# Kernel tuning notes

Measured on AMD Instinct MI355X. Metric: run time of the kernel, lower is better.

The kernel has to match this reference:

```python
import jax, jax.numpy as jnp
import numpy as np

DIM = 128
HEADS = 8
K_RATIO = 0.5
LAYER_SCALE = 0.1
EPS = 1e-6


def setup_inputs() -> dict:
    key = jax.random.key(0)
    ks = jax.random.split(key, 18)
    d = DIM
    hd3 = d * 3  # high-frequency channels (lh,hl,hh)
    f = lambda k, shape, s=0.05: jax.random.normal(k, shape, dtype=jnp.float32) * s
    return {
        "x": jax.random.normal(ks[0], (8, d, 64, 64), dtype=jnp.float32),
        "qkv_w": f(ks[1], (3 * d, d)),
        "proj_w": f(ks[2], (d, d)),
        "attn_gn_g": 1.0 + f(ks[3], (d,)),
        "attn_gn_b": f(ks[4], (d,)),
        "he_dw_w": f(ks[5], (hd3, 1, 3, 3)),
        "he_gn1_g": 1.0 + f(ks[6], (hd3,)),
        "he_gn1_b": f(ks[7], (hd3,)),
        "he_pw_w": f(ks[8], (hd3, hd3)),
        "he_gn2_g": 1.0 + f(ks[9], (hd3,)),
        "he_gn2_b": f(ks[10], (hd3,)),
        "alpha": jnp.array([0.1], dtype=jnp.float32),
        "ffn_w1": f(ks[11], (2 * d, d)),
        "ffn_gn1_g": 1.0 + f(ks[12], (2 * d,)),
        "ffn_gn1_b": f(ks[13], (2 * d,)),
        "ffn_w2": f(ks[14], (d, 2 * d)),
        "ffn_gn2_g": 1.0 + f(ks[15], (d,)),
        "ffn_gn2_b": f(ks[16], (d,)),
    }


def _group_norm(x, g, b, groups):
    B, C, H, W = x.shape
    xg = x.reshape(B, groups, -1)
    mu = xg.mean(-1, keepdims=True)
    var = xg.var(-1, keepdims=True)
    xn = ((xg - mu) * jax.lax.rsqrt(var + EPS)).reshape(B, C, H, W)
    return xn * g[:, None, None] + b[:, None, None]


def _conv1x1(x, w):
    return jnp.einsum('oc,bchw->bohw', w, x)


def _l2norm(t):
    # matches F.normalize(dim=-1, eps=1e-12): x / norm.clamp_min(eps)
    return t / jnp.maximum(jnp.linalg.norm(t, axis=-1, keepdims=True), 1e-12)


def _sparse_attn(ll, qkv_w, proj_w, g, b):
    B, C, H, W = ll.shape
    N = H * W
    nh = HEADS
    hd = C // nh
    scale = hd ** -0.5
    qkv = _conv1x1(ll, qkv_w).reshape(B, 3, nh, hd, N)
    q = jnp.swapaxes(qkv[:, 0], -1, -2)  # [B,nh,N,hd]
    k = jnp.swapaxes(qkv[:, 1], -1, -2)
    v = jnp.swapaxes(qkv[:, 2], -1, -2)
    q = _l2norm(q)
    k = _l2norm(k)
    attn = jnp.einsum('bhnd,bhmd->bhnm', q, k) * scale  # [B,nh,N,N]
    attn = jnp.clip(attn, -32.0, 32.0)  # fp32 clamp value
    k_num = max(int(N * K_RATIO), 1)
    if k_num < N:
        _, idx = jax.lax.top_k(attn, k_num)  # [B,nh,N,k_num]
        flat_attn = attn.reshape(-1, N)
        rows = jnp.arange(flat_attn.shape[0])[:, None]
        mask = jnp.zeros(flat_attn.shape, dtype=bool).at[rows, idx.reshape(-1, k_num)].set(True)
        attn = jnp.where(mask.reshape(attn.shape), attn, jnp.float32(-1e9))
    attn = jax.nn.softmax(attn, axis=-1)
    out = jnp.einsum('bhnm,bhmd->bhnd', attn, v)
    out = jnp.swapaxes(out, 2, 3).reshape(B, C, H, W)
    out = _conv1x1(out, proj_w)
    return _group_norm(out, g, b, min(32, C // 4))


def _high_enhance(h, dw_w, g1, b1, pw_w, g2, b2, alpha):
    C = h.shape[1]
    groups = min(32, C // 8)
    y = jax.lax.conv_general_dilated(
        h, dw_w, window_strides=(1, 1), padding='SAME',
        feature_group_count=C, dimension_numbers=('NCHW', 'OIHW', 'NCHW'))
    y = jax.nn.silu(_group_norm(y, g1, b1, groups))
    y = _group_norm(_conv1x1(y, pw_w), g2, b2, groups)
    return h + alpha[0] * y


def _iwt(ll, lh, hl, hh):
    a = ll - lh - hl + hh  # goes to (even row, even col)
    bq = ll - lh + hl - hh  # (odd row, even col)
    c = ll + lh - hl - hh  # (even row, odd col)
    d = ll + lh + hl + hh  # (odd row, odd col)
    B, C, H, W = ll.shape
    row_even = jnp.stack([a, c], axis=-1)  # [B,C,H,W,2] col parity
    row_odd = jnp.stack([bq, d], axis=-1)
    h = jnp.stack([row_even, row_odd], axis=3)  # [B,C,H,2,W,2]
    return h.reshape(B, C, 2 * H, 2 * W)


def _ffn(x, w1, g1, b1, w2, g2, b2):
    d = x.shape[1]
    groups = min(32, d // 4)
    y = _group_norm(_conv1x1(x, w1), g1, b1, groups)
    y = jax.nn.gelu(y, approximate=False)
    return _group_norm(_conv1x1(y, w2), g2, b2, groups)


def reference(x, qkv_w, proj_w, attn_gn_g, attn_gn_b,
              he_dw_w, he_gn1_g, he_gn1_b, he_pw_w, he_gn2_g, he_gn2_b, alpha,
              ffn_w1, ffn_gn1_g, ffn_gn1_b, ffn_w2, ffn_gn2_g, ffn_gn2_b):
    # DWT (Haar, stride-2 slicing)
    x1 = x[:, :, 0::2, 0::2]
    x2 = x[:, :, 1::2, 0::2]
    x3 = x[:, :, 0::2, 1::2]
    x4 = x[:, :, 1::2, 1::2]
    ll = (x1 + x2 + x3 + x4) * 0.5
    lh = (-x1 - x2 + x3 + x4) * 0.5
    hl = (-x1 + x2 - x3 + x4) * 0.5
    hh = (x1 - x2 - x3 + x4) * 0.5
    high = jnp.concatenate([lh, hl, hh], axis=1)

    ll_out = _sparse_attn(ll, qkv_w, proj_w, attn_gn_g, attn_gn_b)
    high_out = _high_enhance(high, he_dw_w, he_gn1_g, he_gn1_b, he_pw_w, he_gn2_g, he_gn2_b, alpha)

    C = ll.shape[1]
    x_rec = _iwt(ll + ll_out, high_out[:, :C], high_out[:, C:2 * C], high_out[:, 2 * C:])

    out = x + LAYER_SCALE * x_rec
    out = out + LAYER_SCALE * _ffn(out, ffn_w1, ffn_gn1_g, ffn_gn1_b, ffn_w2, ffn_gn2_g, ffn_gn2_b)
    return out
```

## Files before the change

### kernel.cpp

```cpp
#include <hip/hip_runtime.h>
#include <cstdint>
#include <cstddef>

#define BB 8
#define CC 128
#define C3 384
#define HH 64
#define H2 32
#define NPIX 1024
#define N4 4096
#define NHD 8
#define HD 16

typedef _Float16 h2f __attribute__((ext_vector_type(2)));
typedef _Float16 h4f __attribute__((ext_vector_type(4)));
typedef float f4 __attribute__((ext_vector_type(4)));

union U4H { uint4 u; h2f h[4]; };
union H4U { h4f v; h2f h[2]; };

__device__ inline h2f pkrtz(float a, float b) {
  return __builtin_bit_cast(h2f, __builtin_amdgcn_cvt_pkrtz(a, b));
}

__global__ __launch_bounds__(256) void k_dwt(const float* __restrict__ x,
                                             float* __restrict__ ll,
                                             float* __restrict__ high) {
  int idx = blockIdx.x * 256 + threadIdx.x;
  int w = idx & 31, h = (idx >> 5) & 31, c = (idx >> 10) & 127, b = idx >> 17;
  const float* xp = x + ((size_t)(b * CC + c) * HH + 2 * h) * HH + 2 * w;
  float x1 = xp[0];
  float x2 = xp[HH];
  float x3 = xp[1];
  float x4 = xp[HH + 1];
  int n = h * H2 + w;
  ll[(size_t)(b * CC + c) * NPIX + n]              = 0.5f * ( x1 + x2 + x3 + x4);
  high[((size_t)b * C3 + c) * NPIX + n]            = 0.5f * (-x1 - x2 + x3 + x4);
  high[((size_t)b * C3 + CC + c) * NPIX + n]       = 0.5f * (-x1 + x2 - x3 + x4);
  high[((size_t)b * C3 + 2 * CC + c) * NPIX + n]   = 0.5f * ( x1 - x2 - x3 + x4);
}

template <int CIN, int P, int OPT>
__global__ __launch_bounds__(256) void k_conv1x1(const float* __restrict__ in,
                                                 const float* __restrict__ w,
                                                 float* __restrict__ out,
                                                 int Cout, int Npix) {
  int tid = threadIdx.x;
  int n0 = (blockIdx.x * 256 + tid) * P;
  int o0 = blockIdx.y * OPT;
  int b = blockIdx.z;
  const float* inb = in + (size_t)b * CIN * Npix + n0;
  const float* wb = w + (size_t)o0 * CIN;
  float acc[OPT][P];
#pragma unroll
  for (int o = 0; o < OPT; ++o)
#pragma unroll
    for (int p = 0; p < P; ++p) acc[o][p] = 0.f;

  for (int c0 = 0; c0 < CIN; c0 += 8) {
#pragma unroll
    for (int c = 0; c < 8; ++c) {
      float vv[P];
      const float* ip = inb + (size_t)(c0 + c) * Npix;
      if constexpr (P == 4) {
        float4 t = *(const float4*)ip;
        vv[0] = t.x; vv[1] = t.y; vv[2] = t.z; vv[3] = t.w;
      } else if constexpr (P == 2) {
        float2 t = *(const float2*)ip;
        vv[0] = t.x; vv[1] = t.y;
      } else {
        vv[0] = ip[0];
      }
#pragma unroll
      for (int o = 0; o < OPT; ++o) {
        float wc = wb[(size_t)o * CIN + c0 + c];
#pragma unroll
        for (int p = 0; p < P; ++p) acc[o][p] = fmaf(wc, vv[p], acc[o][p]);
      }
    }
  }
  size_t ob = ((size_t)b * Cout + o0) * Npix + n0;
#pragma unroll
  for (int o = 0; o < OPT; ++o) {
    float* op = out + ob + (size_t)o * Npix;
    if constexpr (P == 4) {
      *(float4*)op = make_float4(acc[o][0], acc[o][1], acc[o][2], acc[o][3]);
    } else if constexpr (P == 2) {
      *(float2*)op = make_float2(acc[o][0], acc[o][1]);
    } else {
      op[0] = acc[o][0];
    }
  }
}

__global__ __launch_bounds__(256) void k_qkvnorm(const float* __restrict__ qkv,
                                                 uint4* __restrict__ qh,
                                                 uint4* __restrict__ kh,
                                                 uint16_t* __restrict__ vt) {
  __shared__ uint16_t lds_v[16 * 256];
  int tid = threadIdx.x;
  int idx = blockIdx.x * 256 + tid;
  int n = idx & 1023, h = (idx >> 10) & 7, b = idx >> 13;
  const float* base = qkv + ((size_t)b * C3 + h * HD) * NPIX + n;
  float q[HD], k[HD], vv[HD];
  float sq = 0.f, sk = 0.f;
#pragma unroll
  for (int d = 0; d < HD; ++d) {
    q[d] = base[(size_t)d * NPIX];
    k[d] = base[(size_t)(CC + d) * NPIX];
    vv[d] = base[(size_t)(2 * CC + d) * NPIX];
    sq += q[d] * q[d];
    sk += k[d] * k[d];
  }
  float rq = 1.f / fmaxf(sqrtf(sq), 1e-12f);
  float rk = 1.f / fmaxf(sqrtf(sk), 1e-12f);
#pragma unroll
  for (int g = 0; g < 2; ++g) {
    U4H pq, pk;
#pragma unroll
    for (int d = 0; d < 4; ++d) {
      int e = g * 8 + 2 * d;
      pq.h[d] = pkrtz(q[e] * rq, q[e + 1] * rq);
      pk.h[d] = pkrtz(k[e] * rk, k[e + 1] * rk);
    }
    qh[(size_t)idx * 2 + g] = pq.u;
    kh[(size_t)idx * 2 + g] = pk.u;
  }
#pragma unroll
  for (int d = 0; d < HD; ++d) {
    union { _Float16 f; uint16_t u; } cv;
    cv.f = (_Float16)vv[d];
    lds_v[d * 256 + tid] = cv.u;
  }
  __syncthreads();
  int bh = idx >> 10;
  int n0 = (blockIdx.x * 256) & 1023;
  const uint32_t* ldw = (const uint32_t*)lds_v;
  uint32_t* vtw = (uint32_t*)(vt + (size_t)bh * 16384 + n0);
#pragma unroll
  for (int r = 0; r < 8; ++r) {
    int d = 2 * r + (tid >> 7);
    int c = tid & 127;
    vtw[(size_t)d * 512 + c] = ldw[d * 128 + c];
  }
}

__global__ __launch_bounds__(256) void k_attn(const uint16_t* __restrict__ qh,
                                              const uint16_t* __restrict__ kh,
                                              const uint16_t* __restrict__ vt,
                                              float* __restrict__ attn_out) {
  __shared__ int cnt_lds[12 * 64];
  __shared__ float sum_lds[64];
  __shared__ f4 obuf[4 * 64];
  int tid = threadIdx.x;
  int lane = tid & 63;
  int w = tid >> 6;
  int blk = blockIdx.x;
  int bh = blk >> 6;
  int q0 = (blk & 63) << 4;
  int lm = lane & 15;
  int lg = lane >> 4;
  int b = bh >> 3, h = bh & 7;

  H4U bq;
  bq.v = *(const h4f*)(qh + ((size_t)bh * 1024 + q0 + lm) * 16 + 4 * lg);
  const h2f qsc = {(_Float16)0.25f, (_Float16)0.25f};
  bq.h[0] *= qsc;
  bq.h[1] *= qsc;

  const f4 z = {0.f, 0.f, 0.f, 0.f};
  const uint16_t* kbase = kh + (size_t)bh * 16384 + 4 * lg;
  h2f sc[16][2];
#pragma unroll
  for (int j = 0; j < 16; ++j) {
    int J = (w << 4) | j;
    h4f ak = *(const h4f*)(kbase + (size_t)(16 * J + lm) * 16);
    f4 d = __builtin_amdgcn_mfma_f32_16x16x16f16(ak, bq.v, z, 0, 0, 0);
    sc[j][0] = pkrtz(d[0], d[1]);
    sc[j][1] = pkrtz(d[2], d[3]);
  }

  float lo = -0.26f, hi = 0.26f;
  _Float16 hlo = (_Float16)(-0.26f);
#pragma unroll 1
  for (int it = 0; it < 12; ++it) {
    float mid = 0.5f * (lo + hi);
    _Float16 hm = (_Float16)mid;
    int c = 0;
#pragma unroll
    for (int j = 0; j < 16; ++j) {
      c += (sc[j][0][0] >= hm);
      c += (sc[j][0][1] >= hm);
      c += (sc[j][1][0] >= hm);
      c += (sc[j][1][1] >= hm);
    }
    c += __shfl_xor(c, 16);
    c += __shfl_xor(c, 32);
    if (lg == 0) cnt_lds[it * 64 + lm * 4 + w] = c;
    __syncthreads();
    int4 c4 = *(const int4*)&cnt_lds[it * 64 + lm * 4];
    int ct = (c4.x + c4.y) + (c4.z + c4.w);
    bool ge = (ct >= 512);
    lo = ge ? mid : lo;
    hlo = ge ? hm : hlo;
    hi = ge ? hi : mid;
  }

  float ss = 0.f;
#pragma unroll
  for (int j = 0; j < 16; ++j) {
#pragma unroll
    for (int r = 0; r < 2; ++r) {
      h2f t = sc[j][r];
      float p0 = (t[0] >= hlo) ? __expf((float)t[0]) : 0.f;
      float p1 = (t[1] >= hlo) ? __expf((float)t[1]) : 0.f;
      ss += p0 + p1;
      sc[j][r] = pkrtz(p0, p1);
    }
  }
  ss += __shfl_xor(ss, 16);
  ss += __shfl_xor(ss, 32);
  if (lg == 0) sum_lds[lm * 4 + w] = ss;
  __syncthreads();
  float4 s4 = *(const float4*)&sum_lds[lm * 4];
  float inv = 1.f / ((s4.x + s4.y) + (s4.z + s4.w));

  const uint16_t* vbase = vt + (size_t)bh * 16384 + (size_t)lm * 1024 + 4 * lg;
  f4 acc[2] = {z, z};
#pragma unroll
  for (int j = 0; j < 16; ++j) {
    int J = (w << 4) | j;
    h4f va = *(const h4f*)(vbase + 16 * J);
    H4U pf;
    pf.h[0] = sc[j][0];
    pf.h[1] = sc[j][1];
    acc[j & 1] = __builtin_amdgcn_mfma_f32_16x16x16f16(va, pf.v, acc[j & 1], 0, 0, 0);
  }
  f4 o = acc[0] + acc[1];
  obuf[(w << 6) | lane] = o;
  __syncthreads();
  if (w == 0) {
    f4 t = obuf[lane] + obuf[64 + lane] + obuf[128 + lane] + obuf[192 + lane];
#pragma unroll
    for (int e = 0; e < 4; ++e) {
      int dim = 4 * lg + e;
      attn_out[((size_t)(b * CC + h * HD + dim) * NPIX) + q0 + lm] = t[e] * inv;
    }
  }
}

__global__ __launch_bounds__(256) void k_dwconv(const float* __restrict__ in,
                                                const float* __restrict__ w,
                                                float* __restrict__ out) {
  int n = blockIdx.x * 256 + threadIdx.x;
  int c = blockIdx.y, b = blockIdx.z;
  int i = n >> 5, j = n & 31;
  const float* inb = in + ((size_t)b * C3 + c) * NPIX;
  const float* wc = w + c * 9;
  float acc = 0.f;
#pragma unroll
  for (int di = -1; di <= 1; ++di) {
    int ii = i + di;
    if (ii < 0 || ii > 31) continue;
#pragma unroll
    for (int dj = -1; dj <= 1; ++dj) {
      int jj = j + dj;
      if (jj < 0 || jj > 31) continue;
      acc += inb[ii * 32 + jj] * wc[(di + 1) * 3 + (dj + 1)];
    }
  }
  out[((size_t)b * C3 + c) * NPIX + n] = acc;
}

template <int ACT, bool HAS_RES>
__global__ __launch_bounds__(512) void k_gn(const float* __restrict__ x,
                                            const float* __restrict__ res,
                                            float* __restrict__ out,
                                            const float* __restrict__ gamma,
                                            const float* __restrict__ beta,
                                            const float* __restrict__ alpha_ptr,
                                            float alpha_const,
                                            int chPerGroup, int Npix, int nshift) {
  int g = blockIdx.x & 31, b = blockIdx.x >> 5;
  int Cout = 32 * chPerGroup;
  int elems = chPerGroup * Npix;
  int nv = elems >> 2;
  size_t base = ((size_t)b * Cout + g * chPerGroup) * Npix;
  const float4* xv = (const float4*)(x + base);
  int tid = threadIdx.x;
  float s = 0.f, s2 = 0.f;
  for (int i = tid; i < nv; i += 512) {
    float4 v = xv[i];
    s += v.x + v.y + v.z + v.w;
    s2 += v.x * v.x + v.y * v.y + v.z * v.z + v.w * v.w;
  }
#pragma unroll
  for (int off = 32; off > 0; off >>= 1) {
    s += __shfl_xor(s, off);
    s2 += __shfl_xor(s2, off);
  }
  __shared__ float ls[8], ls2[8];
  int wv = tid >> 6, ln = tid & 63;
  if (ln == 0) { ls[wv] = s; ls2[wv] = s2; }
  __syncthreads();
  float st = 0.f, s2t = 0.f;
#pragma unroll
  for (int i = 0; i < 8; ++i) { st += ls[i]; s2t += ls2[i]; }
  float inv_n = 1.f / (float)elems;
  float mean = st * inv_n;
  float var = s2t * inv_n - mean * mean;
  float rstd = rsqrtf(var + 1e-6f);
  float a = alpha_ptr ? alpha_ptr[0] : alpha_const;
  const float4* rv = (const float4*)(res + base);
  float4* ov = (float4*)(out + base);
  int cshift = nshift - 2;
  for (int i = tid; i < nv; i += 512) {
    float4 v = xv[i];
    int cc = g * chPerGroup + (i >> cshift);
    float gm = gamma[cc], bt = beta[cc];
    float r[4] = {v.x, v.y, v.z, v.w};
#pragma unroll
    for (int p = 0; p < 4; ++p) {
      float gnv = (r[p] - mean) * rstd * gm + bt;
      if (ACT == 1)      r[p] = gnv / (1.f + __expf(-gnv));
      else if (ACT == 2) r[p] = 0.5f * gnv * (1.f + erff(gnv * 0.70710678118654752f));
      else               r[p] = gnv;
    }
    float4 o;
    if (HAS_RES) {
      float4 rr = rv[i];
      o = make_float4(rr.x + a * r[0], rr.y + a * r[1], rr.z + a * r[2], rr.w + a * r[3]);
    } else {
      o = make_float4(r[0], r[1], r[2], r[3]);
    }
    ov[i] = o;
  }
}

__global__ __launch_bounds__(256) void k_iwt(const float* __restrict__ x,
                                             const float* __restrict__ s1,
                                             const float* __restrict__ hout,
                                             float* __restrict__ out) {
  int idx = blockIdx.x * 256 + threadIdx.x;
  int w = idx & 31, h = (idx >> 5) & 31, c = (idx >> 10) & 127, b = idx >> 17;
  int n = h * 32 + w;
  float ll = s1[(size_t)(b * CC + c) * NPIX + n];
  float lh = hout[((size_t)b * C3 + c) * NPIX + n];
  float hl = hout[((size_t)b * C3 + CC + c) * NPIX + n];
  float hh = hout[((size_t)b * C3 + 2 * CC + c) * NPIX + n];
  float va = ll - lh - hl + hh;
  float vb = ll - lh + hl - hh;
  float vc = ll + lh - hl - hh;
  float vd = ll + lh + hl + hh;
  size_t xb = ((size_t)(b * CC + c) * HH + 2 * h) * HH + 2 * w;
  out[xb]          = x[xb]          + 0.1f * va;
  out[xb + 1]      = x[xb + 1]      + 0.1f * vc;
  out[xb + HH]     = x[xb + HH]     + 0.1f * vb;
  out[xb + HH + 1] = x[xb + HH + 1] + 0.1f * vd;
}

extern "C" void kernel_launch(void* const* d_in, const int* in_sizes, int n_in,
                              void* d_out, int out_size, void* d_ws, size_t ws_size,
                              hipStream_t stream) {
  const float* x         = (const float*)d_in[0];
  const float* qkv_w     = (const float*)d_in[1];
  const float* proj_w    = (const float*)d_in[2];
  const float* attn_gn_g = (const float*)d_in[3];
  const float* attn_gn_b = (const float*)d_in[4];
  const float* he_dw_w   = (const float*)d_in[5];
  const float* he_gn1_g  = (const float*)d_in[6];
  const float* he_gn1_b  = (const float*)d_in[7];
  const float* he_pw_w   = (const float*)d_in[8];
  const float* he_gn2_g  = (const float*)d_in[9];
  const float* he_gn2_b  = (const float*)d_in[10];
  const float* alpha     = (const float*)d_in[11];
  const float* ffn_w1    = (const float*)d_in[12];
  const float* ffn_gn1_g = (const float*)d_in[13];
  const float* ffn_gn1_b = (const float*)d_in[14];
  const float* ffn_w2    = (const float*)d_in[15];
  const float* ffn_gn2_g = (const float*)d_in[16];
  const float* ffn_gn2_b = (const float*)d_in[17];
  float* out = (float*)d_out;

  float* ws = (float*)d_ws;
  float* ll   = ws;
  float* high = ws + 1048576;
  float* qkv  = ws + 4194304;
  float* qnkv = ws + 7340032;
  float* atto = ws + 10485760;
  float* proj = ws + 11534336;
  float* f1   = ws + 12582912;
  float* f3   = ws + 20971520;
  uint4* qh = (uint4*)qnkv;
  uint4* kh = (uint4*)(qnkv + 524288);
  uint16_t* vt = (uint16_t*)(qnkv + 1048576);
  float* y1 = qkv;
  float* pw = qnkv;

  k_dwt<<<4096, 256, 0, stream>>>(x, ll, high);
  k_conv1x1<128, 1, 8><<<dim3(4, 48, 8), 256, 0, stream>>>(ll, qkv_w, qkv, 384, 1024);
  k_qkvnorm<<<256, 256, 0, stream>>>(qkv, qh, kh, vt);
  k_attn<<<4096, 256, 0, stream>>>((const uint16_t*)qh, (const uint16_t*)kh, vt, atto);
  k_conv1x1<128, 1, 4><<<dim3(4, 32, 8), 256, 0, stream>>>(atto, proj_w, proj, 128, 1024);
  k_gn<0, true><<<256, 512, 0, stream>>>(proj, ll, proj, attn_gn_g, attn_gn_b,
                                         nullptr, 1.0f, 4, 1024, 10);
  k_dwconv<<<dim3(4, 384, 8), 256, 0, stream>>>(high, he_dw_w, y1);
  k_gn<1, false><<<256, 512, 0, stream>>>(y1, nullptr, y1, he_gn1_g, he_gn1_b,
                                          nullptr, 0.f, 12, 1024, 10);
  k_conv1x1<384, 1, 8><<<dim3(4, 48, 8), 256, 0, stream>>>(y1, he_pw_w, pw, 384, 1024);
  k_gn<0, true><<<256, 512, 0, stream>>>(pw, high, pw, he_gn2_g, he_gn2_b,
                                         alpha, 0.f, 12, 1024, 10);
  k_iwt<<<4096, 256, 0, stream>>>(x, proj, pw, out);
  k_conv1x1<128, 2, 8><<<dim3(8, 32, 8), 256, 0, stream>>>(out, ffn_w1, f1, 256, 4096);
  k_gn<2, false><<<256, 512, 0, stream>>>(f1, nullptr, f1, ffn_gn1_g, ffn_gn1_b,
                                          nullptr, 0.f, 8, 4096, 12);
  k_conv1x1<256, 2, 8><<<dim3(8, 16, 8), 256, 0, stream>>>(f1, ffn_w2, f3, 128, 4096);
  k_gn<0, true><<<256, 512, 0, stream>>>(f3, out, out, ffn_gn2_g, ffn_gn2_b,
                                         nullptr, 0.1f, 4, 4096, 12);
  (void)in_sizes; (void)n_in; (void)out_size; (void)ws_size;
}
```

Measured before the change: 398.5 us.

## Fuse convolutions with group norm and cache GN inputs in registers

The depthwise conv is fused with GroupNorm+SiLU in one kernel that holds a 12-channel group tile in LDS. The high-branch pointwise conv and FFN first conv are fused with their GroupNorm and residual or GELU epilogues, one block per (batch, group), so the separate GN passes and their extra DRAM round trips go away. The remaining GN kernels keep the loaded values in registers instead of reading them twice. The second FFN conv uses a swizzled 1D grid with 4 pixels per thread. The trade-off is only 256 blocks for the fused kernels, each with a large serial channel loop and many registers, which can leave the GPU underoccupied.

```diff
diff --git a/kernel.cpp b/kernel.cpp
--- a/kernel.cpp
+++ b/kernel.cpp
@@ -40,15 +40,24 @@
   high[((size_t)b * C3 + 2 * CC + c) * NPIX + n]   = 0.5f * ( x1 - x2 - x3 + x4);
 }
 
-template <int CIN, int P, int OPT>
+template <int CIN, int P, int OPT, bool SWZ = false>
 __global__ __launch_bounds__(256) void k_conv1x1(const float* __restrict__ in,
                                                  const float* __restrict__ w,
                                                  float* __restrict__ out,
                                                  int Cout, int Npix) {
   int tid = threadIdx.x;
-  int n0 = (blockIdx.x * 256 + tid) * P;
-  int o0 = blockIdx.y * OPT;
-  int b = blockIdx.z;
+  int n0, o0, b;
+  if constexpr (SWZ) {
+    int L = blockIdx.x;
+    int low = L & 31;
+    b = low >> 2;
+    n0 = ((low & 3) * 256 + tid) * P;
+    o0 = (L >> 5) * OPT;
+  } else {
+    n0 = (blockIdx.x * 256 + tid) * P;
+    o0 = blockIdx.y * OPT;
+    b = blockIdx.z;
+  }
   const float* inb = in + (size_t)b * CIN * Npix + n0;
   const float* wb = w + (size_t)o0 * CIN;
   float acc[OPT][P];
@@ -249,48 +258,246 @@
   }
 }
 
-__global__ __launch_bounds__(256) void k_dwconv(const float* __restrict__ in,
-                                                const float* __restrict__ w,
-                                                float* __restrict__ out) {
-  int n = blockIdx.x * 256 + threadIdx.x;
-  int c = blockIdx.y, b = blockIdx.z;
-  int i = n >> 5, j = n & 31;
-  const float* inb = in + ((size_t)b * C3 + c) * NPIX;
-  const float* wc = w + c * 9;
-  float acc = 0.f;
-#pragma unroll
-  for (int di = -1; di <= 1; ++di) {
-    int ii = i + di;
-    if (ii < 0 || ii > 31) continue;
-#pragma unroll
-    for (int dj = -1; dj <= 1; ++dj) {
-      int jj = j + dj;
-      if (jj < 0 || jj > 31) continue;
-      acc += inb[ii * 32 + jj] * wc[(di + 1) * 3 + (dj + 1)];
-    }
-  }
-  out[((size_t)b * C3 + c) * NPIX + n] = acc;
-}
-
-template <int ACT, bool HAS_RES>
-__global__ __launch_bounds__(512) void k_gn(const float* __restrict__ x,
-                                            const float* __restrict__ res,
-                                            float* __restrict__ out,
-                                            const float* __restrict__ gamma,
-                                            const float* __restrict__ beta,
-                                            const float* __restrict__ alpha_ptr,
-                                            float alpha_const,
-                                            int chPerGroup, int Npix, int nshift) {
+__global__ __launch_bounds__(256) void k_dwgn(const float* __restrict__ in,
+                                              const float* __restrict__ w,
+                                              float* __restrict__ out,
+                                              const float* __restrict__ gamma,
+                                              const float* __restrict__ beta) {
+  __shared__ float xs[12 * 1152];
+  __shared__ float sred[4], s2red[4];
+  int blk = blockIdx.x;
+  int b = blk & 7, g = blk >> 3;
+  int tid = threadIdx.x;
+  int c0 = g * 12;
+  const float* inb = in + ((size_t)b * C3 + c0) * NPIX;
+#pragma unroll
+  for (int k = 0; k < 12; ++k) {
+    int e = (k * 256 + tid) * 4;
+    int cc = e >> 10, rem = e & 1023;
+    int row = rem >> 5, col = rem & 31;
+    float4 v = *(const float4*)(inb + e);
+    *(float4*)&xs[cc * 1152 + row * 36 + col] = v;
+  }
+  __syncthreads();
+  int n0 = tid * 4;
+  int i = n0 >> 5, j0 = n0 & 31;
+  float acc[12][4];
+  float s = 0.f, s2 = 0.f;
+#pragma unroll
+  for (int cc = 0; cc < 12; ++cc) {
+    const float* wc = w + (size_t)(c0 + cc) * 9;
+    float w0 = wc[0], w1 = wc[1], w2 = wc[2], w3 = wc[3], w4 = wc[4],
+          w5 = wc[5], w6 = wc[6], w7 = wc[7], w8 = wc[8];
+    float r[3][6];
+#pragma unroll
+    for (int di = 0; di < 3; ++di) {
+      int ii = i + di - 1;
+      bool rv = (ii >= 0 && ii < 32);
+#pragma unroll
+      for (int dj = 0; dj < 6; ++dj) {
+        int jj = j0 + dj - 1;
+        r[di][dj] = (rv && jj >= 0 && jj < 32) ? xs[cc * 1152 + ii * 36 + jj] : 0.f;
+      }
+    }
+#pragma unroll
+    for (int p = 0; p < 4; ++p) {
+      float a = r[0][p] * w0 + r[0][p + 1] * w1 + r[0][p + 2] * w2
+              + r[1][p] * w3 + r[1][p + 1] * w4 + r[1][p + 2] * w5
+              + r[2][p] * w6 + r[2][p + 1] * w7 + r[2][p + 2] * w8;
+      acc[cc][p] = a;
+      s += a;
+      s2 += a * a;
+    }
+  }
+#pragma unroll
+  for (int off = 32; off > 0; off >>= 1) {
+    s += __shfl_xor(s, off);
+    s2 += __shfl_xor(s2, off);
+  }
+  int wv = tid >> 6;
+  if ((tid & 63) == 0) { sred[wv] = s; s2red[wv] = s2; }
+  __syncthreads();
+  float st = sred[0] + sred[1] + sred[2] + sred[3];
+  float s2t = s2red[0] + s2red[1] + s2red[2] + s2red[3];
+  float inv_n = 1.f / 12288.f;
+  float mean = st * inv_n;
+  float var = s2t * inv_n - mean * mean;
+  float rstd = rsqrtf(var + 1e-6f);
+#pragma unroll
+  for (int cc = 0; cc < 12; ++cc) {
+    float gm = gamma[c0 + cc], bt = beta[c0 + cc];
+    float4 o;
+    float* op = (float*)&o;
+#pragma unroll
+    for (int p = 0; p < 4; ++p) {
+      float gnv = (acc[cc][p] - mean) * rstd * gm + bt;
+      op[p] = gnv / (1.f + __expf(-gnv));
+    }
+    *(float4*)(out + ((size_t)b * C3 + c0 + cc) * NPIX + n0) = o;
+  }
+}
+
+__global__ __launch_bounds__(256) void k_pwgn(const float* __restrict__ in,
+                                              const float* __restrict__ w,
+                                              const float* __restrict__ res,
+                                              float* __restrict__ out,
+                                              const float* __restrict__ gamma,
+                                              const float* __restrict__ beta,
+                                              const float* __restrict__ alpha_ptr) {
+  __shared__ float wl[12 * 384];
+  __shared__ float sred[4], s2red[4];
+  int blk = blockIdx.x;
+  int b = blk & 7, g = blk >> 3;
+  int tid = threadIdx.x;
+  int c0 = g * 12;
+  const float* wsrc = w + (size_t)c0 * C3;
+  for (int k = tid; k < 12 * 384; k += 256) wl[k] = wsrc[k];
+  __syncthreads();
+  const float* inb = in + (size_t)b * C3 * NPIX + tid * 4;
+  float acc[12][4];
+#pragma unroll
+  for (int o = 0; o < 12; ++o)
+#pragma unroll
+    for (int p = 0; p < 4; ++p) acc[o][p] = 0.f;
+#pragma unroll 4
+  for (int c = 0; c < 384; ++c) {
+    float4 v = *(const float4*)(inb + (size_t)c * NPIX);
+#pragma unroll
+    for (int o = 0; o < 12; ++o) {
+      float wv = wl[o * 384 + c];
+      acc[o][0] = fmaf(wv, v.x, acc[o][0]);
+      acc[o][1] = fmaf(wv, v.y, acc[o][1]);
+      acc[o][2] = fmaf(wv, v.z, acc[o][2]);
+      acc[o][3] = fmaf(wv, v.w, acc[o][3]);
+    }
+  }
+  float s = 0.f, s2 = 0.f;
+#pragma unroll
+  for (int o = 0; o < 12; ++o)
+#pragma unroll
+    for (int p = 0; p < 4; ++p) { s += acc[o][p]; s2 += acc[o][p] * acc[o][p]; }
+#pragma unroll
+  for (int off = 32; off > 0; off >>= 1) {
+    s += __shfl_xor(s, off);
+    s2 += __shfl_xor(s2, off);
+  }
+  int wv = tid >> 6;
+  if ((tid & 63) == 0) { sred[wv] = s; s2red[wv] = s2; }
+  __syncthreads();
+  float st = sred[0] + sred[1] + sred[2] + sred[3];
+  float s2t = s2red[0] + s2red[1] + s2red[2] + s2red[3];
+  float inv_n = 1.f / 12288.f;
+  float mean = st * inv_n;
+  float var = s2t * inv_n - mean * mean;
+  float rstd = rsqrtf(var + 1e-6f);
+  float a = alpha_ptr[0];
+#pragma unroll
+  for (int o = 0; o < 12; ++o) {
+    float gm = gamma[c0 + o], bt = beta[c0 + o];
+    size_t base = ((size_t)b * C3 + c0 + o) * NPIX + tid * 4;
+    float4 rr = *(const float4*)(res + base);
+    float4 ov;
+    ov.x = rr.x + a * ((acc[o][0] - mean) * rstd * gm + bt);
+    ov.y = rr.y + a * ((acc[o][1] - mean) * rstd * gm + bt);
+    ov.z = rr.z + a * ((acc[o][2] - mean) * rstd * gm + bt);
+    ov.w = rr.w + a * ((acc[o][3] - mean) * rstd * gm + bt);
+    *(float4*)(out + base) = ov;
+  }
+}
+
+__global__ __launch_bounds__(512) void k_ffn1(const float* __restrict__ in,
+                                              const float* __restrict__ w,
+                                              float* __restrict__ out,
+                                              const float* __restrict__ gamma,
+                                              const float* __restrict__ beta) {
+  __shared__ float wl[8 * 128];
+  __shared__ float sred[8], s2red[8];
+  int blk = blockIdx.x;
+  int b = blk & 7, g = blk >> 3;
+  int tid = threadIdx.x;
+  int c0 = g * 8;
+  const float* wsrc = w + (size_t)c0 * CC;
+  for (int k = tid; k < 8 * 128; k += 512) wl[k] = wsrc[k];
+  __syncthreads();
+  const float* inb = in + (size_t)b * CC * N4 + tid * 8;
+  float acc[8][8];
+#pragma unroll
+  for (int o = 0; o < 8; ++o)
+#pragma unroll
+    for (int p = 0; p < 8; ++p) acc[o][p] = 0.f;
+#pragma unroll 4
+  for (int c = 0; c < 128; ++c) {
+    const float* ip = inb + (size_t)c * N4;
+    float4 v0 = *(const float4*)ip;
+    float4 v1 = *(const float4*)(ip + 4);
+#pragma unroll
+    for (int o = 0; o < 8; ++o) {
+      float wv = wl[o * 128 + c];
+      acc[o][0] = fmaf(wv, v0.x, acc[o][0]);
+      acc[o][1] = fmaf(wv, v0.y, acc[o][1]);
+      acc[o][2] = fmaf(wv, v0.z, acc[o][2]);
+      acc[o][3] = fmaf(wv, v0.w, acc[o][3]);
+      acc[o][4] = fmaf(wv, v1.x, acc[o][4]);
+      acc[o][5] = fmaf(wv, v1.y, acc[o][5]);
+      acc[o][6] = fmaf(wv, v1.z, acc[o][6]);
+      acc[o][7] = fmaf(wv, v1.w, acc[o][7]);
+    }
+  }
+  float s = 0.f, s2 = 0.f;
+#pragma unroll
+  for (int o = 0; o < 8; ++o)
+#pragma unroll
+    for (int p = 0; p < 8; ++p) { s += acc[o][p]; s2 += acc[o][p] * acc[o][p]; }
+#pragma unroll
+  for (int off = 32; off > 0; off >>= 1) {
+    s += __shfl_xor(s, off);
+    s2 += __shfl_xor(s2, off);
+  }
+  int wv = tid >> 6;
+  if ((tid & 63) == 0) { sred[wv] = s; s2red[wv] = s2; }
+  __syncthreads();
+  float st = 0.f, s2t = 0.f;
+#pragma unroll
+  for (int k = 0; k < 8; ++k) { st += sred[k]; s2t += s2red[k]; }
+  float inv_n = 1.f / 32768.f;
+  float mean = st * inv_n;
+  float var = s2t * inv_n - mean * mean;
+  float rstd = rsqrtf(var + 1e-6f);
+#pragma unroll
+  for (int o = 0; o < 8; ++o) {
+    float gm = gamma[c0 + o], bt = beta[c0 + o];
+    float r[8];
+#pragma unroll
+    for (int p = 0; p < 8; ++p) {
+      float gnv = (acc[o][p] - mean) * rstd * gm + bt;
+      r[p] = 0.5f * gnv * (1.f + erff(gnv * 0.70710678118654752f));
+    }
+    float* op = out + ((size_t)(b * 256 + c0 + o)) * N4 + tid * 8;
+    *(float4*)op = make_float4(r[0], r[1], r[2], r[3]);
+    *(float4*)(op + 4) = make_float4(r[4], r[5], r[6], r[7]);
+  }
+}
+
+template <int ITER, int ACT, bool HAS_RES>
+__global__ __launch_bounds__(512) void k_gnr(const float* __restrict__ x,
+                                             const float* __restrict__ res,
+                                             float* __restrict__ out,
+                                             const float* __restrict__ gamma,
+                                             const float* __restrict__ beta,
+                                             float alpha_const,
+                                             int chPerGroup, int Npix, int nshift) {
   int g = blockIdx.x & 31, b = blockIdx.x >> 5;
   int Cout = 32 * chPerGroup;
   int elems = chPerGroup * Npix;
-  int nv = elems >> 2;
   size_t base = ((size_t)b * Cout + g * chPerGroup) * Npix;
   const float4* xv = (const float4*)(x + base);
   int tid = threadIdx.x;
+  float4 xc[ITER];
   float s = 0.f, s2 = 0.f;
-  for (int i = tid; i < nv; i += 512) {
-    float4 v = xv[i];
+#pragma unroll
+  for (int k = 0; k < ITER; ++k) {
+    float4 v = xv[tid + k * 512];
+    xc[k] = v;
     s += v.x + v.y + v.z + v.w;
     s2 += v.x * v.x + v.y * v.y + v.z * v.z + v.w * v.w;
   }
@@ -305,19 +512,20 @@
   __syncthreads();
   float st = 0.f, s2t = 0.f;
 #pragma unroll
-  for (int i = 0; i < 8; ++i) { st += ls[i]; s2t += ls2[i]; }
+  for (int k = 0; k < 8; ++k) { st += ls[k]; s2t += ls2[k]; }
   float inv_n = 1.f / (float)elems;
   float mean = st * inv_n;
   float var = s2t * inv_n - mean * mean;
   float rstd = rsqrtf(var + 1e-6f);
-  float a = alpha_ptr ? alpha_ptr[0] : alpha_const;
   const float4* rv = (const float4*)(res + base);
   float4* ov = (float4*)(out + base);
   int cshift = nshift - 2;
-  for (int i = tid; i < nv; i += 512) {
-    float4 v = xv[i];
+#pragma unroll
+  for (int k = 0; k < ITER; ++k) {
+    int i = tid + k * 512;
     int cc = g * chPerGroup + (i >> cshift);
     float gm = gamma[cc], bt = beta[cc];
+    float4 v = xc[k];
     float r[4] = {v.x, v.y, v.z, v.w};
 #pragma unroll
     for (int p = 0; p < 4; ++p) {
@@ -329,7 +537,8 @@
     float4 o;
     if (HAS_RES) {
       float4 rr = rv[i];
-      o = make_float4(rr.x + a * r[0], rr.y + a * r[1], rr.z + a * r[2], rr.w + a * r[3]);
+      o = make_float4(rr.x + alpha_const * r[0], rr.y + alpha_const * r[1],
+                      rr.z + alpha_const * r[2], rr.w + alpha_const * r[3]);
     } else {
       o = make_float4(r[0], r[1], r[2], r[3]);
     }
@@ -402,20 +611,14 @@
   k_qkvnorm<<<256, 256, 0, stream>>>(qkv, qh, kh, vt);
   k_attn<<<4096, 256, 0, stream>>>((const uint16_t*)qh, (const uint16_t*)kh, vt, atto);
   k_conv1x1<128, 1, 4><<<dim3(4, 32, 8), 256, 0, stream>>>(atto, proj_w, proj, 128, 1024);
-  k_gn<0, true><<<256, 512, 0, stream>>>(proj, ll, proj, attn_gn_g, attn_gn_b,
-                                         nullptr, 1.0f, 4, 1024, 10);
-  k_dwconv<<<dim3(4, 384, 8), 256, 0, stream>>>(high, he_dw_w, y1);
-  k_gn<1, false><<<256, 512, 0, stream>>>(y1, nullptr, y1, he_gn1_g, he_gn1_b,
-                                          nullptr, 0.f, 12, 1024, 10);
-  k_conv1x1<384, 1, 8><<<dim3(4, 48, 8), 256, 0, stream>>>(y1, he_pw_w, pw, 384, 1024);
-  k_gn<0, true><<<256, 512, 0, stream>>>(pw, high, pw, he_gn2_g, he_gn2_b,
-                                         alpha, 0.f, 12, 1024, 10);
+  k_gnr<2, 0, true><<<256, 512, 0, stream>>>(proj, ll, proj, attn_gn_g, attn_gn_b,
+                                             1.0f, 4, 1024, 10);
+  k_dwgn<<<256, 256, 0, stream>>>(high, he_dw_w, y1, he_gn1_g, he_gn1_b);
+  k_pwgn<<<256, 256, 0, stream>>>(y1, he_pw_w, high, pw, he_gn2_g, he_gn2_b, alpha);
   k_iwt<<<4096, 256, 0, stream>>>(x, proj, pw, out);
-  k_conv1x1<128, 2, 8><<<dim3(8, 32, 8), 256, 0, stream>>>(out, ffn_w1, f1, 256, 4096);
-  k_gn<2, false><<<256, 512, 0, stream>>>(f1, nullptr, f1, ffn_gn1_g, ffn_gn1_b,
-                                          nullptr, 0.f, 8, 4096, 12);
-  k_conv1x1<256, 2, 8><<<dim3(8, 16, 8), 256, 0, stream>>>(f1, ffn_w2, f3, 128, 4096);
-  k_gn<0, true><<<256, 512, 0, stream>>>(f3, out, out, ffn_gn2_g, ffn_gn2_b,
-                                         nullptr, 0.1f, 4, 4096, 12);
+  k_ffn1<<<256, 512, 0, stream>>>(out, ffn_w1, f1, ffn_gn1_g, ffn_gn1_b);
+  k_conv1x1<256, 4, 8, true><<<512, 256, 0, stream>>>(f1, ffn_w2, f3, 128, 4096);
+  k_gnr<8, 0, true><<<256, 512, 0, stream>>>(f3, out, out, ffn_gn2_g, ffn_gn2_b,
+                                             0.1f, 4, 4096, 12);
   (void)in_sizes; (void)n_in; (void)out_size; (void)ws_size;
 }
```

After: 383.1 us. 1.04x faster.
